# Performance work log

Hardware: AMD Instinct MI355X
Metric: run time of the kernel (lower is better)

## Reference

```python
import jax, jax.numpy as jnp
import numpy as np
import math

D = 1024      # input/embed dim
H = 16        # heads
HD = D // H   # head dim
FF = 4096     # feedforward dim
B, S = 2, 2048
LN_EPS = 1e-5
NEG = -9e15


def setup_inputs() -> dict:
    key = jax.random.key(0)
    ks = jax.random.split(key, 16)
    inp = {
        "x": jax.random.normal(ks[0], (B, S, D), jnp.float32),
        "mask": jax.random.randint(ks[1], (1, 1, S, S), 0, 2, jnp.int32),
        "pos_bias": jax.random.normal(ks[2], (1, H, S, S), jnp.float32),
        "sinusoidal_pos": jax.random.normal(ks[3], (1, 1, S, HD), jnp.float32),
        # params (xavier-ish scale)
        "Wqkv": jax.random.normal(ks[4], (D, 3 * D), jnp.float32) * math.sqrt(2.0 / (D + 3 * D)),
        "bqkv": jnp.zeros((3 * D,), jnp.float32),
        "Wo": jax.random.normal(ks[5], (D, D), jnp.float32) * math.sqrt(1.0 / D),
        "bo": jnp.zeros((D,), jnp.float32),
        "W1": jax.random.normal(ks[6], (D, FF), jnp.float32) * math.sqrt(2.0 / (D + FF)),
        "b1": jnp.zeros((FF,), jnp.float32),
        "W2": jax.random.normal(ks[7], (FF, D), jnp.float32) * math.sqrt(2.0 / (D + FF)),
        "b2": jnp.zeros((D,), jnp.float32),
        "g1": jnp.ones((D,), jnp.float32),
        "be1": jnp.zeros((D,), jnp.float32),
        "g2": jnp.ones((D,), jnp.float32),
        "be2": jnp.zeros((D,), jnp.float32),
    }
    return inp


def _layernorm(x, g, b):
    mu = jnp.mean(x, axis=-1, keepdims=True)
    var = jnp.mean(jnp.square(x - mu), axis=-1, keepdims=True)
    return (x - mu) * jax.lax.rsqrt(var + LN_EPS) * g + b


def _rotate_half(x):
    # x: [..., HD] -> reshape [..., 2, HD//2], swap with negation, concat
    r = x.reshape(*x.shape[:-1], 2, -1)
    x1, x2 = r[..., 0, :], r[..., 1, :]
    return jnp.concatenate([-x2, x1], axis=-1)


def _rope(x, sp):
    # sp: [1,1,S,HD]; x: [B,H,S,HD]
    return x * jnp.cos(sp) + _rotate_half(x) * jnp.sin(sp)


def reference(x, mask, pos_bias, sinusoidal_pos, Wqkv, bqkv, Wo, bo,
              W1, b1, W2, b2, g1, be1, g2, be2):
    # pre-norm (note: residual uses the normalized x, matching the source)
    x = _layernorm(x, g1, be1)
    b, s, d = x.shape
    qkv = (x @ Wqkv + bqkv).reshape(b, s, H, 3 * HD).transpose(0, 2, 1, 3)
    q, k, v = jnp.split(qkv, 3, axis=-1)  # each [B,H,S,HD]
    sp = sinusoidal_pos[:, :, -s:]
    q = _rope(q, sp)
    k = _rope(k, sp)
    logits = jnp.einsum("bhqd,bhkd->bhqk", q, k)
    logits = (logits + pos_bias) / math.sqrt(HD)
    logits = jnp.where(mask == 0, NEG, logits)
    attn = jax.nn.softmax(logits, axis=-1)
    vals = jnp.einsum("bhqk,bhkd->bhqd", attn, v)
    vals = vals.transpose(0, 2, 1, 3).reshape(b, s, d)
    attn_out = vals @ Wo + bo
    x = x + attn_out
    x = _layernorm(x, g2, be2)
    h = jax.nn.gelu(x @ W1 + b1, approximate=False)  # torch GELU is exact
    x = x + (h @ W2 + b2)
    return x
```

## Files before the change

kernel.cpp:

```cpp
#include <hip/hip_runtime.h>
#include <math.h>

#define DD   1024
#define HH   16
#define HDD  64
#define FFF  4096
#define NB   2
#define NS   2048
#define NR   (NB * NS)
#define TDQ  (3 * DD)
#define NKT  (NS / 64)
#define NSP  2

typedef __attribute__((ext_vector_type(8))) _Float16 hfrag;
typedef __attribute__((ext_vector_type(4))) _Float16 h4v;
typedef __attribute__((ext_vector_type(16))) float f32x16;
typedef __attribute__((ext_vector_type(8))) unsigned short us8;
typedef __attribute__((ext_vector_type(4))) unsigned int u32x4;

__device__ __forceinline__ float4 ld4(const float* p) {
    return *reinterpret_cast<const float4*>(p);
}
__device__ __forceinline__ float gelu_f(float x) {
    return 0.5f * x * (1.0f + erff(x * 0.70710678118654752440f));
}
#define MFMA32H(a, b, c) __builtin_amdgcn_mfma_f32_32x32x16_f16((a), (b), (c), 0, 0, 0)

__global__ __launch_bounds__(256) void ln_kernel(const float* __restrict__ in,
        const float* __restrict__ gw, const float* __restrict__ bw,
        float* __restrict__ outf, _Float16* __restrict__ oh) {
    int row = blockIdx.x;
    float4 v = reinterpret_cast<const float4*>(in + (size_t)row * DD)[threadIdx.x];
    float s1 = v.x + v.y + v.z + v.w;
    float s2 = v.x * v.x + v.y * v.y + v.z * v.z + v.w * v.w;
#pragma unroll
    for (int off = 1; off < 64; off <<= 1) {
        s1 += __shfl_xor(s1, off);
        s2 += __shfl_xor(s2, off);
    }
    __shared__ float r1[4], r2[4];
    int wid = threadIdx.x >> 6;
    if ((threadIdx.x & 63) == 0) { r1[wid] = s1; r2[wid] = s2; }
    __syncthreads();
    s1 = r1[0] + r1[1] + r1[2] + r1[3];
    s2 = r2[0] + r2[1] + r2[2] + r2[3];
    float mu   = s1 * (1.0f / DD);
    float var  = s2 * (1.0f / DD) - mu * mu;
    float rstd = rsqrtf(var + 1e-5f);
    float4 g = reinterpret_cast<const float4*>(gw)[threadIdx.x];
    float4 b = reinterpret_cast<const float4*>(bw)[threadIdx.x];
    float o[4];
    o[0] = (v.x - mu) * rstd * g.x + b.x;
    o[1] = (v.y - mu) * rstd * g.y + b.y;
    o[2] = (v.z - mu) * rstd * g.z + b.z;
    o[3] = (v.w - mu) * rstd * g.w + b.w;
    float4 of; of.x = o[0]; of.y = o[1]; of.z = o[2]; of.w = o[3];
    reinterpret_cast<float4*>(outf + (size_t)row * DD)[threadIdx.x] = of;
    h4v hv;
#pragma unroll
    for (int j = 0; j < 4; ++j) hv[j] = (_Float16)o[j];
    *reinterpret_cast<h4v*>(oh + (size_t)row * DD + threadIdx.x * 4) = hv;
}

__global__ __launch_bounds__(256) void wt_convert(const float* __restrict__ W,
        _Float16* __restrict__ Th, int K, int N) {
    __shared__ float s[32][33];
    int tx = threadIdx.x & 31, ty = threadIdx.x >> 5;
    int n0 = blockIdx.x * 32, k0 = blockIdx.y * 32;
#pragma unroll
    for (int i = 0; i < 4; ++i)
        s[ty + i * 8][tx] = W[(size_t)(k0 + ty + i * 8) * N + n0 + tx];
    __syncthreads();
#pragma unroll
    for (int i = 0; i < 4; ++i) {
        int n = n0 + ty + i * 8;
        Th[(size_t)n * K + k0 + tx] = (_Float16)s[tx][ty + i * 8];
    }
}

__global__ __launch_bounds__(256) void cs4_table(const float* __restrict__ sp,
        h4v* __restrict__ cs4) {
    int i = blockIdx.x * 256 + threadIdx.x;
    int s = i >> 5, d = i & 31;
    float a = sp[s * 64 + d], b = sp[s * 64 + d + 32];
    h4v v;
    v[0] = (_Float16)cosf(a); v[1] = (_Float16)sinf(a);
    v[2] = (_Float16)cosf(b); v[3] = (_Float16)sinf(b);
    cs4[i] = v;
}

__global__ __launch_bounds__(256) void mask8(const int* __restrict__ mask,
        unsigned char* __restrict__ mb) {
    int i = blockIdx.x * 256 + threadIdx.x;
    int4 v = reinterpret_cast<const int4*>(mask)[i];
    unsigned int o = (unsigned int)(v.x & 1) | ((unsigned int)(v.y & 1) << 8)
                   | ((unsigned int)(v.z & 1) << 16) | ((unsigned int)(v.w & 1) << 24);
    reinterpret_cast<unsigned int*>(mb)[i] = o;
}

__global__ __launch_bounds__(256) void vtrans(const _Float16* __restrict__ Vr,
        _Float16* __restrict__ Vt) {
    __shared__ _Float16 sv[64][72];
    const int t = threadIdx.x;
    const int tile = blockIdx.x, bh = blockIdx.y;
    const int r = t >> 2, p = t & 3;
    const _Float16* src = Vr + ((size_t)bh * NS + tile * 64 + r) * HDD;
    hfrag v0 = *reinterpret_cast<const hfrag*>(src + p * 16);
    hfrag v1 = *reinterpret_cast<const hfrag*>(src + p * 16 + 8);
#pragma unroll
    for (int j = 0; j < 8; ++j) {
        sv[p * 16 + j][r]     = v0[j];
        sv[p * 16 + 8 + j][r] = v1[j];
    }
    __syncthreads();
    {
        int d = t >> 2, kb = (t & 3) * 16;
        size_t obase = ((size_t)bh * HDD + d) * NS + tile * 64 + kb;
        *reinterpret_cast<hfrag*>(Vt + obase)     = *reinterpret_cast<hfrag*>(&sv[d][kb]);
        *reinterpret_cast<hfrag*>(Vt + obase + 8) = *reinterpret_cast<hfrag*>(&sv[d][kb + 8]);
    }
}

__global__ __launch_bounds__(256) void attn_mfma(
        const _Float16* __restrict__ Qp, const _Float16* __restrict__ Kp,
        const _Float16* __restrict__ Vt,
        const float* __restrict__ pos_bias, const unsigned char* __restrict__ maskb,
        float* __restrict__ Opart, float2* __restrict__ Lpart) {
    __shared__ _Float16 kT[2][64][72];
    __shared__ _Float16 vT[2][64][72];
    __shared__ _Float16 PBs[4][32][68];
    const int t = threadIdx.x;
    const int w = t >> 6, lane = t & 63, lq = lane & 31, hi = lane >> 5;
    const int h = blockIdx.y;
    const int qt = blockIdx.x, sp = blockIdx.z;
    const int q0 = qt * 128;
    const int qg = q0 + 32 * w + lq;
    const int sw = ((lq >> 3) & 3) << 3;
    const int KT0 = sp * (NKT / NSP), KT1 = KT0 + (NKT / NSP);
    const float C1  = 0.18033688011112042f;
    const float THR = 11.5f;

    hfrag qf[2][4];
#pragma unroll
    for (int bt = 0; bt < 2; ++bt)
#pragma unroll
        for (int dk = 0; dk < 4; ++dk)
            qf[bt][dk] = *reinterpret_cast<const hfrag*>(
                Qp + ((size_t)(bt * HH + h) * NS + qg) * HDD + 16 * dk + 8 * hi);

    f32x16 o[2][2];
#pragma unroll
    for (int bt = 0; bt < 2; ++bt) { o[bt][0] = (f32x16)0.0f; o[bt][1] = (f32x16)0.0f; }
    float mrun[2] = { -INFINITY, -INFINITY }, lsum[2] = { 0.0f, 0.0f };

    const int sr0 = t >> 2, sc = t & 3;
    const int swr = ((sr0 >> 3) & 3) << 3;
    const int brow = lane >> 4;
    const int bcol = (lane & 15) * 4;
    us8 kr[2][2], vr[2][2];
    float4 pbr[8]; unsigned int pmk[8];

#define STAGE_LOAD(KT) {                                                        \
        int kv0_ = (KT) * 64;                                                   \
        _Pragma("unroll")                                                       \
        for (int bt = 0; bt < 2; ++bt) {                                        \
            size_t kb_ = ((size_t)(bt * HH + h) * NS + kv0_ + sr0) * HDD + 16 * sc; \
            size_t vb_ = ((size_t)(bt * HH + h) * HDD + sr0) * NS + kv0_ + 16 * sc; \
            kr[bt][0] = *reinterpret_cast<const us8*>(Kp + kb_);                \
            kr[bt][1] = *reinterpret_cast<const us8*>(Kp + kb_ + 8);            \
            vr[bt][0] = *reinterpret_cast<const us8*>(Vt + vb_);                \
            vr[bt][1] = *reinterpret_cast<const us8*>(Vt + vb_ + 8);            \
        }                                                                       \
        _Pragma("unroll")                                                       \
        for (int i = 0; i < 8; ++i) {                                           \
            int rg_ = q0 + 32 * w + brow + 4 * i;                               \
            pbr[i] = ld4(pos_bias + ((size_t)h * NS + rg_) * NS + kv0_ + bcol); \
            pmk[i] = *reinterpret_cast<const unsigned int*>(                    \
                         maskb + (size_t)rg_ * NS + kv0_ + bcol);               \
        }                                                                       \
    }

    STAGE_LOAD(KT0);
    for (int kt = KT0; kt < KT1; ++kt) {
        __syncthreads();
#pragma unroll
        for (int bt = 0; bt < 2; ++bt) {
            *reinterpret_cast<us8*>(&kT[bt][sr0][(16 * sc) ^ swr])     = kr[bt][0];
            *reinterpret_cast<us8*>(&kT[bt][sr0][(16 * sc + 8) ^ swr]) = kr[bt][1];
            *reinterpret_cast<us8*>(&vT[bt][sr0][(16 * sc) ^ swr])     = vr[bt][0];
            *reinterpret_cast<us8*>(&vT[bt][sr0][(16 * sc + 8) ^ swr]) = vr[bt][1];
        }
#pragma unroll
        for (int i = 0; i < 8; ++i) {
            h4v pv;
#pragma unroll
            for (int j = 0; j < 4; ++j)
                pv[j] = ((pmk[i] >> (8 * j)) & 0xffu)
                      ? (_Float16)(pbr[i][j] * C1) : (_Float16)(-60000.0f);
            *reinterpret_cast<h4v*>(&PBs[w][brow + 4 * i][bcol]) = pv;
        }
        __syncthreads();
        if (kt + 1 < KT1) STAGE_LOAD(kt + 1);

        f32x16 sS[2][2];
#pragma unroll
        for (int bt = 0; bt < 2; ++bt) {
            sS[bt][0] = (f32x16)0.0f; sS[bt][1] = (f32x16)0.0f;
#pragma unroll
            for (int dk = 0; dk < 4; ++dk) {
                hfrag k0 = *reinterpret_cast<const hfrag*>(
                    &kT[bt][lq][(16 * dk + 8 * hi) ^ sw]);
                hfrag k1 = *reinterpret_cast<const hfrag*>(
                    &kT[bt][32 + lq][(16 * dk + 8 * hi) ^ sw]);
                sS[bt][0] = MFMA32H(k0, qf[bt][dk], sS[bt][0]);
                sS[bt][1] = MFMA32H(k1, qf[bt][dk], sS[bt][1]);
            }
        }
#pragma unroll
        for (int bt = 0; bt < 2; ++bt) {
            float sv[2][16];
#pragma unroll
            for (int m2 = 0; m2 < 2; ++m2)
#pragma unroll
                for (int g = 0; g < 4; ++g) {
                    h4v pb4 = *reinterpret_cast<const h4v*>(
                        &PBs[w][lq][32 * m2 + 8 * g + 4 * hi]);
#pragma unroll
                    for (int j = 0; j < 4; ++j) {
                        int r = 4 * g + j;
                        sv[m2][r] = fmaf(sS[bt][m2][r], C1, (float)pb4[j]);
                    }
                }
            float mx = sv[0][0];
#pragma unroll
            for (int m2 = 0; m2 < 2; ++m2)
#pragma unroll
                for (int r = 0; r < 16; ++r) mx = fmaxf(mx, sv[m2][r]);
            mx = fmaxf(mx, __shfl_xor(mx, 32));
            if (__any(mx > mrun[bt] + THR)) {
                float mnew = fmaxf(mrun[bt], mx);
                float corr = __builtin_amdgcn_exp2f(mrun[bt] - mnew);
                lsum[bt] *= corr;
                mrun[bt] = mnew;
#pragma unroll
                for (int r = 0; r < 16; ++r) {
                    int iq = (r & 3) + 8 * (r >> 2) + 4 * hi;
                    float cr = __shfl(corr, iq);
                    o[bt][0][r] *= cr; o[bt][1][r] *= cr;
                }
            }
            float ps = 0.0f;
            hfrag af[4];
#pragma unroll
            for (int m2 = 0; m2 < 2; ++m2)
#pragma unroll
                for (int gp = 0; gp < 2; ++gp) {
                    float p0 = __builtin_amdgcn_exp2f(sv[m2][8 * gp + 0] - mrun[bt]);
                    float p1 = __builtin_amdgcn_exp2f(sv[m2][8 * gp + 1] - mrun[bt]);
                    float p2 = __builtin_amdgcn_exp2f(sv[m2][8 * gp + 2] - mrun[bt]);
                    float p3 = __builtin_amdgcn_exp2f(sv[m2][8 * gp + 3] - mrun[bt]);
                    float p4 = __builtin_amdgcn_exp2f(sv[m2][8 * gp + 4] - mrun[bt]);
                    float p5 = __builtin_amdgcn_exp2f(sv[m2][8 * gp + 5] - mrun[bt]);
                    float p6 = __builtin_amdgcn_exp2f(sv[m2][8 * gp + 6] - mrun[bt]);
                    float p7 = __builtin_amdgcn_exp2f(sv[m2][8 * gp + 7] - mrun[bt]);
                    ps += (p0 + p1) + (p2 + p3) + (p4 + p5) + (p6 + p7);
                    unsigned int XA = __builtin_bit_cast(unsigned int, __builtin_amdgcn_cvt_pkrtz(p0, p1));
                    unsigned int XB = __builtin_bit_cast(unsigned int, __builtin_amdgcn_cvt_pkrtz(p2, p3));
                    unsigned int XC = __builtin_bit_cast(unsigned int, __builtin_amdgcn_cvt_pkrtz(p4, p5));
                    unsigned int XD = __builtin_bit_cast(unsigned int, __builtin_amdgcn_cvt_pkrtz(p6, p7));
                    unsigned int YA = (unsigned int)__shfl_xor((int)XA, 32);
                    unsigned int YB = (unsigned int)__shfl_xor((int)XB, 32);
                    unsigned int YC = (unsigned int)__shfl_xor((int)XC, 32);
                    unsigned int YD = (unsigned int)__shfl_xor((int)XD, 32);
                    u32x4 aw;
                    aw[0] = hi ? YC : XA;
                    aw[1] = hi ? YD : XB;
                    aw[2] = hi ? XC : YA;
                    aw[3] = hi ? XD : YB;
                    af[m2 * 2 + gp] = __builtin_bit_cast(hfrag, aw);
                }
            ps += __shfl_xor(ps, 32);
            lsum[bt] += ps;
#pragma unroll
            for (int kp = 0; kp < 4; ++kp) {
                hfrag v0 = *reinterpret_cast<const hfrag*>(
                    &vT[bt][lq][(16 * kp + 8 * hi) ^ sw]);
                hfrag v1 = *reinterpret_cast<const hfrag*>(
                    &vT[bt][32 + lq][(16 * kp + 8 * hi) ^ sw]);
                o[bt][0] = MFMA32H(af[kp], v0, o[bt][0]);
                o[bt][1] = MFMA32H(af[kp], v1, o[bt][1]);
            }
        }
    }
#undef STAGE_LOAD
#pragma unroll
    for (int bt = 0; bt < 2; ++bt) {
        size_t obase = (((size_t)((bt * HH + h) * 16 + qt)) * NSP + sp) * (size_t)(128 * 64);
#pragma unroll
        for (int r = 0; r < 16; ++r) {
            int iq = (r & 3) + 8 * (r >> 2) + 4 * hi;
            Opart[obase + (size_t)(32 * w + iq) * 64 + lq]      = o[bt][0][r];
            Opart[obase + (size_t)(32 * w + iq) * 64 + 32 + lq] = o[bt][1][r];
        }
        if (hi == 0) {
            float2 ml; ml.x = mrun[bt]; ml.y = lsum[bt];
            Lpart[(((size_t)((bt * HH + h) * 16 + qt)) * NSP + sp) * 128 + 32 * w + lq] = ml;
        }
    }
}

__global__ __launch_bounds__(256) void attn_combine(const float* __restrict__ Opart,
        const float2* __restrict__ Lpart, _Float16* __restrict__ valf) {
    const int qt = blockIdx.x;
    const int h = blockIdx.y >> 1, b = blockIdx.y & 1;
    const int bh = b * HH + h;
    const int t = threadIdx.x;
    const int qloc = t >> 2, d0 = (t & 3) * 16;
    size_t base = ((size_t)(bh * 16 + qt)) * NSP;
#pragma unroll
    for (int half = 0; half < 2; ++half) {
        int q = qloc + 64 * half;
        float2 ml0 = Lpart[(base + 0) * 128 + q];
        float2 ml1 = Lpart[(base + 1) * 128 + q];
        float m = fmaxf(ml0.x, ml1.x);
        float a0 = __builtin_amdgcn_exp2f(ml0.x - m);
        float a1 = __builtin_amdgcn_exp2f(ml1.x - m);
        float inv = 1.0f / (ml0.y * a0 + ml1.y * a1);
        const float* O0 = Opart + (base + 0) * 8192 + (size_t)q * 64 + d0;
        const float* O1 = Opart + (base + 1) * 8192 + (size_t)q * 64 + d0;
        _Float16* dst = valf + ((size_t)(b * NS + qt * 128 + q)) * DD + h * HDD + d0;
#pragma unroll
        for (int j = 0; j < 4; ++j) {
            float4 x0 = ld4(O0 + 4 * j), x1 = ld4(O1 + 4 * j);
            h4v o;
            o[0] = (_Float16)((x0.x * a0 + x1.x * a1) * inv);
            o[1] = (_Float16)((x0.y * a0 + x1.y * a1) * inv);
            o[2] = (_Float16)((x0.z * a0 + x1.z * a1) * inv);
            o[3] = (_Float16)((x0.w * a0 + x1.w * a1) * inv);
            *reinterpret_cast<h4v*>(dst + 4 * j) = o;
        }
    }
}

template<int EPI>
__global__ __launch_bounds__(256, 2) void gemm_h(
        const _Float16* __restrict__ A, const _Float16* __restrict__ B,
        const float* __restrict__ bias, const float* __restrict__ resid,
        float* __restrict__ Cf, _Float16* __restrict__ Ch,
        _Float16* __restrict__ Qp, _Float16* __restrict__ Kp,
        _Float16* __restrict__ Vr, const h4v* __restrict__ cs4,
        int M, int N, int K) {
    __shared__ _Float16 sA[128][72];
    __shared__ _Float16 sB[128][72];
    const int t = threadIdx.x;
    const int w = t >> 6, lane = t & 63, lq = lane & 31, hi = lane >> 5;
    const int wr = w >> 1, wc = w & 1;
    const int m0 = blockIdx.y * 128, n0 = blockIdx.x * 128;
    const int sw = ((lq >> 3) & 3) << 3;

    f32x16 acc[2][2];
#pragma unroll
    for (int m = 0; m < 2; ++m)
#pragma unroll
        for (int n = 0; n < 2; ++n) acc[m][n] = (f32x16)0.0f;

    const int sr = t >> 1, skc = (t & 1) * 16;
    const int swr = ((sr >> 3) & 3) << 3;
    const _Float16* Ap = A + (size_t)(m0 + sr) * K + skc;
    const _Float16* Bp = B + (size_t)(n0 + sr) * K + skc;

    for (int k0 = 0; k0 < K; k0 += 32) {
        us8 a0 = *reinterpret_cast<const us8*>(Ap + k0);
        us8 a1 = *reinterpret_cast<const us8*>(Ap + k0 + 8);
        us8 b0 = *reinterpret_cast<const us8*>(Bp + k0);
        us8 b1 = *reinterpret_cast<const us8*>(Bp + k0 + 8);
        __syncthreads();
        *reinterpret_cast<us8*>(&sA[sr][(skc) ^ swr])     = a0;
        *reinterpret_cast<us8*>(&sA[sr][(skc + 8) ^ swr]) = a1;
        *reinterpret_cast<us8*>(&sB[sr][(skc) ^ swr])     = b0;
        *reinterpret_cast<us8*>(&sB[sr][(skc + 8) ^ swr]) = b1;
        __syncthreads();
        hfrag fa[2][2], fb[2][2];
#pragma unroll
        for (int mb = 0; mb < 2; ++mb)
#pragma unroll
            for (int kc = 0; kc < 2; ++kc)
                fa[mb][kc] = *reinterpret_cast<const hfrag*>(
                    &sA[wr * 64 + mb * 32 + lq][(kc * 16 + 8 * hi) ^ sw]);
#pragma unroll
        for (int nb = 0; nb < 2; ++nb)
#pragma unroll
            for (int kc = 0; kc < 2; ++kc)
                fb[nb][kc] = *reinterpret_cast<const hfrag*>(
                    &sB[wc * 64 + nb * 32 + lq][(kc * 16 + 8 * hi) ^ sw]);
#pragma unroll
        for (int kc = 0; kc < 2; ++kc)
#pragma unroll
            for (int mb = 0; mb < 2; ++mb)
#pragma unroll
                for (int nb = 0; nb < 2; ++nb)
                    acc[mb][nb] = MFMA32H(fa[mb][kc], fb[nb][kc], acc[mb][nb]);
    }
    if (EPI == 4) {
        const int b64 = blockIdx.x * 2 + wc;
        const int qk = b64 % 3, hh = b64 / 3;
        const float bv0 = bias[n0 + wc * 64 + lq];
        const float bv1 = bias[n0 + wc * 64 + 32 + lq];
#pragma unroll
        for (int mb = 0; mb < 2; ++mb)
#pragma unroll
            for (int g = 0; g < 4; ++g)
#pragma unroll
                for (int rr = 0; rr < 4; ++rr) {
                    int r = 4 * g + rr;
                    int rowg = m0 + wr * 64 + mb * 32 + rr + 8 * g + 4 * hi;
                    int s = rowg & (NS - 1), bb = rowg >> 11;
                    float v0 = acc[mb][0][r] + bv0;
                    float v1 = acc[mb][1][r] + bv1;
                    _Float16* dstb = (qk == 0 ? Qp : (qk == 1 ? Kp : Vr))
                        + ((size_t)(bb * HH + hh) * NS + s) * HDD;
                    if (qk < 2) {
                        h4v cs = cs4[(size_t)s * 32 + lq];
                        float c1 = (float)cs[0], s1 = (float)cs[1];
                        float c2 = (float)cs[2], s2 = (float)cs[3];
                        dstb[lq]      = (_Float16)(v0 * c1 - v1 * s1);
                        dstb[32 + lq] = (_Float16)(v1 * c2 + v0 * s2);
                    } else {
                        dstb[lq]      = (_Float16)v0;
                        dstb[32 + lq] = (_Float16)v1;
                    }
                }
        return;
    }
#pragma unroll
    for (int mb = 0; mb < 2; ++mb)
#pragma unroll
        for (int nb = 0; nb < 2; ++nb) {
            int colg = n0 + wc * 64 + nb * 32 + lq;
            float bv = bias[colg];
#pragma unroll
            for (int r = 0; r < 16; ++r) {
                int rowg = m0 + wr * 64 + mb * 32 + (r & 3) + 8 * (r >> 2) + 4 * hi;
                float v = acc[mb][nb][r] + bv;
                if (EPI == 1) v += resid[(size_t)rowg * N + colg];
                if (EPI == 2) {
                    Ch[(size_t)rowg * N + colg] = (_Float16)gelu_f(v);
                } else {
                    Cf[(size_t)rowg * N + colg] = v;
                }
            }
        }
}

__global__ __launch_bounds__(256, 2) void gemm_h2(
        const _Float16* __restrict__ A, const _Float16* __restrict__ B,
        const float* __restrict__ bias, const float* __restrict__ resid,
        float* __restrict__ Cf, int M, int N, int K) {
    __shared__ _Float16 sA[64][72];
    __shared__ _Float16 sB[128][72];
    const int t = threadIdx.x;
    const int w = t >> 6, lane = t & 63, lq = lane & 31, hi = lane >> 5;
    const int m0 = blockIdx.y * 64, n0 = blockIdx.x * 128;
    const int sw = ((lq >> 3) & 3) << 3;

    f32x16 acc[2];
    acc[0] = (f32x16)0.0f; acc[1] = (f32x16)0.0f;

    const int ar = t >> 2, akc = (t & 3) * 8;
    const int aswr = ((ar >> 3) & 3) << 3;
    const int br = t >> 1, bkc = (t & 1) * 16;
    const int bswr = ((br >> 3) & 3) << 3;
    const _Float16* Ap = A + (size_t)(m0 + ar) * K + akc;
    const _Float16* Bp = B + (size_t)(n0 + br) * K + bkc;

    for (int k0 = 0; k0 < K; k0 += 32) {
        us8 a0 = *reinterpret_cast<const us8*>(Ap + k0);
        us8 b0 = *reinterpret_cast<const us8*>(Bp + k0);
        us8 b1 = *reinterpret_cast<const us8*>(Bp + k0 + 8);
        __syncthreads();
        *reinterpret_cast<us8*>(&sA[ar][(akc) ^ aswr])     = a0;
        *reinterpret_cast<us8*>(&sB[br][(bkc) ^ bswr])     = b0;
        *reinterpret_cast<us8*>(&sB[br][(bkc + 8) ^ bswr]) = b1;
        __syncthreads();
        hfrag fa[2][2], fb[2];
#pragma unroll
        for (int mb = 0; mb < 2; ++mb)
#pragma unroll
            for (int kc = 0; kc < 2; ++kc)
                fa[mb][kc] = *reinterpret_cast<const hfrag*>(
                    &sA[mb * 32 + lq][(kc * 16 + 8 * hi) ^ sw]);
#pragma unroll
        for (int kc = 0; kc < 2; ++kc)
            fb[kc] = *reinterpret_cast<const hfrag*>(
                &sB[32 * w + lq][(kc * 16 + 8 * hi) ^ sw]);
#pragma unroll
        for (int kc = 0; kc < 2; ++kc)
#pragma unroll
            for (int mb = 0; mb < 2; ++mb)
                acc[mb] = MFMA32H(fa[mb][kc], fb[kc], acc[mb]);
    }
    int colg = n0 + 32 * w + lq;
    float bv = bias[colg];
#pragma unroll
    for (int mb = 0; mb < 2; ++mb)
#pragma unroll
        for (int r = 0; r < 16; ++r) {
            int rowg = m0 + mb * 32 + (r & 3) + 8 * (r >> 2) + 4 * hi;
            float v = acc[mb][r] + bv + resid[(size_t)rowg * N + colg];
            Cf[(size_t)rowg * N + colg] = v;
        }
}

extern "C" void kernel_launch(void* const* d_in, const int* in_sizes, int n_in,
                              void* d_out, int out_size, void* d_ws, size_t ws_size,
                              hipStream_t stream) {
    const float* x        = (const float*)d_in[0];
    const int*   mask     = (const int*)d_in[1];
    const float* pos_bias = (const float*)d_in[2];
    const float* sp       = (const float*)d_in[3];
    const float* Wqkv     = (const float*)d_in[4];
    const float* bqkv     = (const float*)d_in[5];
    const float* Wo       = (const float*)d_in[6];
    const float* bo       = (const float*)d_in[7];
    const float* W1       = (const float*)d_in[8];
    const float* b1       = (const float*)d_in[9];
    const float* W2       = (const float*)d_in[10];
    const float* b2       = (const float*)d_in[11];
    const float* g1       = (const float*)d_in[12];
    const float* be1      = (const float*)d_in[13];
    const float* g2       = (const float*)d_in[14];
    const float* be2      = (const float*)d_in[15];
    float* out = (float*)d_out;
    char* wsb = (char*)d_ws;

    float*          xbuf  = (float*)(wsb);
    _Float16*       actF  = (_Float16*)(wsb + ((size_t)16 << 20));
    _Float16*       wT    = (_Float16*)(wsb + ((size_t)24 << 20));
    h4v*            cs4   = (h4v*)(wsb + ((size_t)32 << 20));
    unsigned char*  mkb   = (unsigned char*)(wsb + ((size_t)34 << 20));
    _Float16*       Vr    = (_Float16*)(wsb + ((size_t)48 << 20));
    _Float16*       Qp    = (_Float16*)(wsb + ((size_t)72 << 20));
    _Float16*       Kp    = (_Float16*)(wsb + ((size_t)80 << 20));
    _Float16*       Vt    = (_Float16*)(wsb + ((size_t)88 << 20));
    _Float16*       hF    = (_Float16*)(wsb + ((size_t)48 << 20));
    float*          Opart = (float*)(wsb + ((size_t)96 << 20));
    float2*         Lpart = (float2*)(wsb + ((size_t)130 << 20));

    ln_kernel<<<NR, 256, 0, stream>>>(x, g1, be1, xbuf, actF);
    cs4_table<<<(NS * 32) / 256, 256, 0, stream>>>(sp, cs4);
    mask8<<<(NS * NS / 4) / 256, 256, 0, stream>>>(mask, mkb);
    wt_convert<<<dim3(TDQ / 32, DD / 32), 256, 0, stream>>>(Wqkv, wT, DD, TDQ);
    gemm_h<4><<<dim3(TDQ / 128, NR / 128), 256, 0, stream>>>(
        actF, wT, bqkv, nullptr, nullptr, nullptr, Qp, Kp, Vr, cs4, NR, TDQ, DD);
    vtrans<<<dim3(NS / 64, NB * HH), 256, 0, stream>>>(Vr, Vt);
    attn_mfma<<<dim3(NS / 128, HH, NSP), 256, 0, stream>>>(
        Qp, Kp, Vt, pos_bias, mkb, Opart, Lpart);
    attn_combine<<<dim3(NS / 128, NB * HH), 256, 0, stream>>>(Opart, Lpart, actF);
    wt_convert<<<dim3(DD / 32, DD / 32), 256, 0, stream>>>(Wo, wT, DD, DD);
    gemm_h2<<<dim3(DD / 128, NR / 64), 256, 0, stream>>>(
        actF, wT, bo, xbuf, xbuf, NR, DD, DD);
    ln_kernel<<<NR, 256, 0, stream>>>(xbuf, g2, be2, xbuf, actF);
    wt_convert<<<dim3(FFF / 32, DD / 32), 256, 0, stream>>>(W1, wT, DD, FFF);
    gemm_h<2><<<dim3(FFF / 128, NR / 128), 256, 0, stream>>>(
        actF, wT, b1, nullptr, nullptr, hF, nullptr, nullptr, nullptr, nullptr,
        NR, FFF, DD);
    wt_convert<<<dim3(DD / 32, FFF / 32), 256, 0, stream>>>(W2, wT, FFF, DD);
    gemm_h2<<<dim3(DD / 128, NR / 64), 256, 0, stream>>>(
        hF, wT, b2, xbuf, out, NR, DD, FFF);
}
```

Before: 405.3 us.

## Double-buffer LDS tiles and prefetch global loads in fp16 GEMM kernels

Both GEMM kernels now keep two LDS tile buffers. The next tile's global loads are issued two steps ahead and written to the alternate buffer while MFMAs run on the current one. This drops one of the two barriers per k-step and hides global load latency behind compute. In exchange, LDS usage doubles and more registers stay live, which could cut occupancy at launch_bounds(256,2).

After: 420.3 us. 3.7% more time.

```diff
diff --git a/kernel.cpp b/kernel.cpp
--- a/kernel.cpp
+++ b/kernel.cpp
@@ -350,8 +350,8 @@
         _Float16* __restrict__ Qp, _Float16* __restrict__ Kp,
         _Float16* __restrict__ Vr, const h4v* __restrict__ cs4,
         int M, int N, int K) {
-    __shared__ _Float16 sA[128][72];
-    __shared__ _Float16 sB[128][72];
+    __shared__ _Float16 sA[2][128][72];
+    __shared__ _Float16 sB[2][128][72];
     const int t = threadIdx.x;
     const int w = t >> 6, lane = t & 63, lq = lane & 31, hi = lane >> 5;
     const int wr = w >> 1, wc = w & 1;
@@ -369,30 +369,40 @@
     const _Float16* Ap = A + (size_t)(m0 + sr) * K + skc;
     const _Float16* Bp = B + (size_t)(n0 + sr) * K + skc;
 
+    us8 a0, a1, b0, b1;
+#define GEMM_LOAD(KOFF) {                                         \
+        a0 = *reinterpret_cast<const us8*>(Ap + (KOFF));          \
+        a1 = *reinterpret_cast<const us8*>(Ap + (KOFF) + 8);      \
+        b0 = *reinterpret_cast<const us8*>(Bp + (KOFF));          \
+        b1 = *reinterpret_cast<const us8*>(Bp + (KOFF) + 8);      \
+    }
+#define GEMM_WRITE(BUF) {                                                   \
+        *reinterpret_cast<us8*>(&sA[BUF][sr][(skc) ^ swr])     = a0;        \
+        *reinterpret_cast<us8*>(&sA[BUF][sr][(skc + 8) ^ swr]) = a1;        \
+        *reinterpret_cast<us8*>(&sB[BUF][sr][(skc) ^ swr])     = b0;        \
+        *reinterpret_cast<us8*>(&sB[BUF][sr][(skc + 8) ^ swr]) = b1;        \
+    }
+    GEMM_LOAD(0);
+    GEMM_WRITE(0);
+    GEMM_LOAD(32);
+    __syncthreads();
+    int cur = 0;
     for (int k0 = 0; k0 < K; k0 += 32) {
-        us8 a0 = *reinterpret_cast<const us8*>(Ap + k0);
-        us8 a1 = *reinterpret_cast<const us8*>(Ap + k0 + 8);
-        us8 b0 = *reinterpret_cast<const us8*>(Bp + k0);
-        us8 b1 = *reinterpret_cast<const us8*>(Bp + k0 + 8);
-        __syncthreads();
-        *reinterpret_cast<us8*>(&sA[sr][(skc) ^ swr])     = a0;
-        *reinterpret_cast<us8*>(&sA[sr][(skc + 8) ^ swr]) = a1;
-        *reinterpret_cast<us8*>(&sB[sr][(skc) ^ swr])     = b0;
-        *reinterpret_cast<us8*>(&sB[sr][(skc + 8) ^ swr]) = b1;
-        __syncthreads();
         hfrag fa[2][2], fb[2][2];
 #pragma unroll
         for (int mb = 0; mb < 2; ++mb)
 #pragma unroll
             for (int kc = 0; kc < 2; ++kc)
                 fa[mb][kc] = *reinterpret_cast<const hfrag*>(
-                    &sA[wr * 64 + mb * 32 + lq][(kc * 16 + 8 * hi) ^ sw]);
+                    &sA[cur][wr * 64 + mb * 32 + lq][(kc * 16 + 8 * hi) ^ sw]);
 #pragma unroll
         for (int nb = 0; nb < 2; ++nb)
 #pragma unroll
             for (int kc = 0; kc < 2; ++kc)
                 fb[nb][kc] = *reinterpret_cast<const hfrag*>(
-                    &sB[wc * 64 + nb * 32 + lq][(kc * 16 + 8 * hi) ^ sw]);
+                    &sB[cur][wc * 64 + nb * 32 + lq][(kc * 16 + 8 * hi) ^ sw]);
+        if (k0 + 32 < K) GEMM_WRITE(cur ^ 1);
+        if (k0 + 64 < K) GEMM_LOAD(k0 + 64);
 #pragma unroll
         for (int kc = 0; kc < 2; ++kc)
 #pragma unroll
@@ -400,7 +410,11 @@
 #pragma unroll
                 for (int nb = 0; nb < 2; ++nb)
                     acc[mb][nb] = MFMA32H(fa[mb][kc], fb[nb][kc], acc[mb][nb]);
-    }
+        __syncthreads();
+        cur ^= 1;
+    }
+#undef GEMM_LOAD
+#undef GEMM_WRITE
     if (EPI == 4) {
         const int b64 = blockIdx.x * 2 + wc;
         const int qk = b64 % 3, hh = b64 / 3;
@@ -456,8 +470,8 @@
         const _Float16* __restrict__ A, const _Float16* __restrict__ B,
         const float* __restrict__ bias, const float* __restrict__ resid,
         float* __restrict__ Cf, int M, int N, int K) {
-    __shared__ _Float16 sA[64][72];
-    __shared__ _Float16 sB[128][72];
+    __shared__ _Float16 sA[2][64][72];
+    __shared__ _Float16 sB[2][128][72];
     const int t = threadIdx.x;
     const int w = t >> 6, lane = t & 63, lq = lane & 31, hi = lane >> 5;
     const int m0 = blockIdx.y * 64, n0 = blockIdx.x * 128;
@@ -473,32 +487,46 @@
     const _Float16* Ap = A + (size_t)(m0 + ar) * K + akc;
     const _Float16* Bp = B + (size_t)(n0 + br) * K + bkc;
 
+    us8 a0, b0, b1;
+#define GEMM2_LOAD(KOFF) {                                        \
+        a0 = *reinterpret_cast<const us8*>(Ap + (KOFF));          \
+        b0 = *reinterpret_cast<const us8*>(Bp + (KOFF));          \
+        b1 = *reinterpret_cast<const us8*>(Bp + (KOFF) + 8);      \
+    }
+#define GEMM2_WRITE(BUF) {                                                  \
+        *reinterpret_cast<us8*>(&sA[BUF][ar][(akc) ^ aswr])     = a0;       \
+        *reinterpret_cast<us8*>(&sB[BUF][br][(bkc) ^ bswr])     = b0;       \
+        *reinterpret_cast<us8*>(&sB[BUF][br][(bkc + 8) ^ bswr]) = b1;       \
+    }
+    GEMM2_LOAD(0);
+    GEMM2_WRITE(0);
+    GEMM2_LOAD(32);
+    __syncthreads();
+    int cur = 0;
     for (int k0 = 0; k0 < K; k0 += 32) {
-        us8 a0 = *reinterpret_cast<const us8*>(Ap + k0);
-        us8 b0 = *reinterpret_cast<const us8*>(Bp + k0);
-        us8 b1 = *reinterpret_cast<const us8*>(Bp + k0 + 8);
-        __syncthreads();
-        *reinterpret_cast<us8*>(&sA[ar][(akc) ^ aswr])     = a0;
-        *reinterpret_cast<us8*>(&sB[br][(bkc) ^ bswr])     = b0;
-        *reinterpret_cast<us8*>(&sB[br][(bkc + 8) ^ bswr]) = b1;
-        __syncthreads();
         hfrag fa[2][2], fb[2];
 #pragma unroll
         for (int mb = 0; mb < 2; ++mb)
 #pragma unroll
             for (int kc = 0; kc < 2; ++kc)
                 fa[mb][kc] = *reinterpret_cast<const hfrag*>(
-                    &sA[mb * 32 + lq][(kc * 16 + 8 * hi) ^ sw]);
+                    &sA[cur][mb * 32 + lq][(kc * 16 + 8 * hi) ^ sw]);
 #pragma unroll
         for (int kc = 0; kc < 2; ++kc)
             fb[kc] = *reinterpret_cast<const hfrag*>(
-                &sB[32 * w + lq][(kc * 16 + 8 * hi) ^ sw]);
+                &sB[cur][32 * w + lq][(kc * 16 + 8 * hi) ^ sw]);
+        if (k0 + 32 < K) GEMM2_WRITE(cur ^ 1);
+        if (k0 + 64 < K) GEMM2_LOAD(k0 + 64);
 #pragma unroll
         for (int kc = 0; kc < 2; ++kc)
 #pragma unroll
             for (int mb = 0; mb < 2; ++mb)
                 acc[mb] = MFMA32H(fa[mb][kc], fb[kc], acc[mb]);
-    }
+        __syncthreads();
+        cur ^= 1;
+    }
+#undef GEMM2_LOAD
+#undef GEMM2_WRITE
     int colg = n0 + 32 * w + lq;
     float bv = bias[colg];
 #pragma unroll
```
